# Kernel tuning notes

Hardware: AMD Instinct MI355X
Metric: run time of the kernel (lower is better)

The kernel has to match this reference:

```python
import jax, jax.numpy as jnp
import numpy as np
from jax import lax

# sign binarization to {-1,+1} with straight-through estimator (standard BNN binarizePM1)
@jax.custom_vjp
def binarize(x):
    return jnp.where(x >= 0, 1.0, -1.0).astype(x.dtype)

def _bin_fwd(x):
    return binarize(x), None

def _bin_bwd(_, g):
    return (g,)  # straight-through

binarize.defvjp(_bin_fwd, _bin_bwd)

def conv2d(x, w, b):
    # NCHW, OIHW, 3x3, stride 1, pad 1
    y = lax.conv_general_dilated(x, w, window_strides=(1, 1), padding=((1, 1), (1, 1)),
                                 dimension_numbers=('NCHW', 'OIHW', 'NCHW'))
    return y + b[None, :, None, None]

def maxpool2(x):
    return lax.reduce_window(x, -jnp.inf, lax.max, (1, 1, 2, 2), (1, 1, 2, 2), 'VALID')

def bn(x, gamma, beta, mean, var, eps=1e-5):
    # inference-mode batchnorm; broadcasts over channel axis 1 (4D) or feature axis 1 (2D)
    if x.ndim == 4:
        shp = (1, -1, 1, 1)
    else:
        shp = (1, -1)
    inv = gamma * lax.rsqrt(var + eps)
    return x * inv.reshape(shp) + (beta - mean * inv).reshape(shp)

def setup_inputs() -> dict:
    key = jax.random.key(0)
    ks = jax.random.split(key, 16)
    B = 4096
    d = {}
    d['x'] = jax.random.normal(ks[0], (B, 1, 28, 28), jnp.float32)
    d['conv1_w'] = jax.random.normal(ks[1], (64, 1, 3, 3), jnp.float32) * 0.1
    d['conv1_b'] = jax.random.normal(ks[2], (64,), jnp.float32) * 0.01
    d['conv2_w'] = jax.random.normal(ks[3], (64, 64, 3, 3), jnp.float32) * 0.05
    d['conv2_b'] = jax.random.normal(ks[4], (64,), jnp.float32) * 0.01
    d['fc1_w'] = jax.random.normal(ks[5], (2048, 7 * 7 * 64), jnp.float32) * 0.02
    d['fc1_b'] = jax.random.normal(ks[6], (2048,), jnp.float32) * 0.01
    d['fc2_w'] = jax.random.normal(ks[7], (10, 2048), jnp.float32) * 0.02
    d['fc2_b'] = jax.random.normal(ks[8], (10,), jnp.float32) * 0.01
    for i, (name, c) in enumerate([('bn1', 64), ('bn2', 64), ('bn3', 2048)]):
        d[name + '_gamma'] = jnp.ones((c,), jnp.float32)
        d[name + '_beta'] = jnp.zeros((c,), jnp.float32)
        d[name + '_mean'] = jax.random.normal(ks[9 + i], (c,), jnp.float32) * 0.1
        d[name + '_var'] = jax.random.uniform(ks[12 + i], (c,), jnp.float32, 0.5, 1.5)
    d['scale'] = jnp.array([1e-5], jnp.float32)
    return d

def reference(x, conv1_w, conv1_b, conv2_w, conv2_b, fc1_w, fc1_b, fc2_w, fc2_b,
              bn1_gamma, bn1_beta, bn1_mean, bn1_var,
              bn2_gamma, bn2_beta, bn2_mean, bn2_var,
              bn3_gamma, bn3_beta, bn3_mean, bn3_var, scale):
    h = conv2d(x, binarize(conv1_w), conv1_b)          # [B,64,28,28]
    h = maxpool2(h)                                    # [B,64,14,14]
    h = bn(h, bn1_gamma, bn1_beta, bn1_mean, bn1_var)
    h = jnp.clip(h, -1.0, 1.0)                         # hardtanh
    h = binarize(h)                                    # qact1
    h = conv2d(h, binarize(conv2_w), conv2_b)          # [B,64,14,14]
    h = maxpool2(h)                                    # [B,64,7,7]
    h = bn(h, bn2_gamma, bn2_beta, bn2_mean, bn2_var)
    h = jnp.clip(h, -1.0, 1.0)
    h = binarize(h)
    h = h.reshape(h.shape[0], -1)                      # [B,3136]
    h = h @ binarize(fc1_w).T + fc1_b                  # [B,2048]
    h = bn(h, bn3_gamma, bn3_beta, bn3_mean, bn3_var)
    h = jnp.clip(h, -1.0, 1.0)
    h = binarize(h)
    h = h @ binarize(fc2_w).T + fc2_b                  # [B,10]
    return h * scale
```

## Files before the change

kernel.cpp:

```cpp
#include <hip/hip_runtime.h>
#include <stdint.h>

typedef unsigned long long ULL;

__global__ __launch_bounds__(256) void prep_small(const float* __restrict__ w1,
        const float* __restrict__ w2, const float* __restrict__ fc2w,
        float* __restrict__ sgn1, ULL* __restrict__ wb2, ULL* __restrict__ wbf2) {
    int wave = threadIdx.x >> 6, lane = threadIdx.x & 63;
    int W = blockIdx.x * 4 + wave;
    if (W < 576) {
        int co = W / 9, tap = W - co * 9;
        ULL wd = __ballot(w2[(co * 64 + lane) * 9 + tap] >= 0.f);
        if (lane == 0) wb2[W] = wd;
    } else if (W < 896) {
        int idx = W - 576;
        int n = idx >> 5, k = idx & 31;
        ULL wd = __ballot(fc2w[n * 2048 + k * 64 + lane] >= 0.f);
        if (lane == 0) wbf2[idx] = wd;
    } else if (W < 905) {
        int i = (W - 896) * 64 + lane;
        if (i < 576) sgn1[i] = (w1[i] >= 0.f) ? 1.f : -1.f;
    }
}

__global__ __launch_bounds__(256) void prep_pack_fc1(const float* __restrict__ fc1w,
                                                     ULL* __restrict__ wbT) {
    __shared__ float rows[4 * 3136];
    int t = threadIdx.x;
    const float* src = fc1w + (size_t)blockIdx.x * 4 * 3136;
    for (int i = t; i < 4 * 3136; i += 256) rows[i] = src[i];
    __syncthreads();
    int wave = t >> 6, lane = t & 63;
    int n = blockIdx.x * 4 + wave;
    const float* r = rows + wave * 3136 + lane * 49;
    for (int p = 0; p < 49; ++p) {
        ULL wd = __ballot(r[p] >= 0.f);
        if (lane == 0) wbT[p * 2048 + n] = wd;
    }
}

__global__ __launch_bounds__(448, 4) void k1_conv1(const float* __restrict__ x,
        const float* __restrict__ sgn1, const float* __restrict__ b1,
        const float* __restrict__ g, const float* __restrict__ be,
        const float* __restrict__ mu, const float* __restrict__ va,
        ULL* __restrict__ qact1) {
    __shared__ float limg[30 * 30];
    int b = blockIdx.x, t = threadIdx.x;
    int wave = t >> 6, lane = t & 63;
    for (int i = t; i < 900; i += 448) limg[i] = 0.f;
    __syncthreads();
    const float* xb = x + (size_t)b * 784;
    for (int i = t; i < 784; i += 448) {
        int y = i / 28, xx = i - y * 28;
        limg[(xx + 1) * 30 + (y + 1)] = xb[i];
    }
    float w[9];
    #pragma unroll
    for (int k = 0; k < 9; ++k) w[k] = sgn1[lane * 9 + k];
    double iv = (double)g[lane] / sqrt((double)va[lane] + 1e-5);
    double cd = (double)be[lane] - (double)mu[lane] * iv;
    double bd = (double)b1[lane];
    __syncthreads();

    #pragma unroll
    for (int rr = 0; rr < 2; ++rr) {
        int py = wave + rr * 7;
        const float* base = &limg[2 * py];
        #pragma unroll
        for (int px = 0; px < 14; ++px) {
            float a00 = 0.f, a01 = 0.f, a10 = 0.f, a11 = 0.f;
            #pragma unroll
            for (int ky = 0; ky < 3; ++ky) {
                #pragma unroll
                for (int kx = 0; kx < 3; ++kx) {
                    float sv = w[ky * 3 + kx];
                    a00 = fmaf(base[(2 * px + kx)     * 30 + ky],     sv, a00);
                    a01 = fmaf(base[(2 * px + kx + 1) * 30 + ky],     sv, a01);
                    a10 = fmaf(base[(2 * px + kx)     * 30 + ky + 1], sv, a10);
                    a11 = fmaf(base[(2 * px + kx + 1) * 30 + ky + 1], sv, a11);
                }
            }
            float m = fmaxf(fmaxf(a00, a01), fmaxf(a10, a11));
            double v  = (double)m + bd;
            double tt = v * iv + cd;
            ULL word = __ballot(tt >= 0.0);
            if (lane == 0) qact1[(size_t)b * 196 + py * 14 + px] = word;
        }
    }
}

__global__ __launch_bounds__(256, 1) void k2_conv2(const ULL* __restrict__ qact1,
        const ULL* __restrict__ wb2, const float* __restrict__ b2,
        const float* __restrict__ g, const float* __restrict__ be,
        const float* __restrict__ mu, const float* __restrict__ va,
        ULL* __restrict__ qact2) {
    int lane = threadIdx.x & 63;
    int s = blockIdx.x * 4 + (threadIdx.x >> 6);

    ULL wk[9];
    #pragma unroll
    for (int k = 0; k < 9; ++k) wk[k] = wb2[lane * 9 + k];
    int pw[9];
    #pragma unroll
    for (int k = 0; k < 9; ++k) pw[k] = 64 - 2 * (int)__popcll(wk[k]);

    double iv   = (double)g[lane] / sqrt((double)va[lane] + 1e-5);
    double cc   = (double)be[lane] - (double)mu[lane] * iv;
    double bias = (double)b2[lane];
    int am, thr;
    if (iv > 0.0) {
        double t0 = -cc / iv - bias;
        int c = (t0 < -590.0) ? -590 : (t0 > 590.0 ? 590 : (int)floor(t0) - 2);
        if (c < -590) c = -590;
        while (c <= 590 && !(((double)c + bias) * iv + cc >= 0.0)) ++c;
        am = 1; thr = c;
    } else if (iv < 0.0) {
        double t0 = -cc / iv - bias;
        int c = (t0 > 590.0) ? 590 : (t0 < -590.0 ? -590 : (int)ceil(t0) + 2);
        if (c > 590) c = 590;
        while (c >= -590 && !(((double)c + bias) * iv + cc >= 0.0)) --c;
        am = -1; thr = c;
    } else {
        am = 1; thr = (cc >= 0.0) ? -1000000 : 1000000;
    }
    int athr = am * thr;

    int cLs = pw[0] + pw[3] + pw[6], cRs = pw[2] + pw[5] + pw[8];
    int rT  = pw[0] + pw[1] + pw[2], rB  = pw[6] + pw[7] + pw[8];
    int tL = cLs + rT - pw[0], tM = rT, tR = cRs + rT - pw[2];
    int bL = cLs + rB - pw[6], bM = rB, bR = cRs + rB - pw[8];

    const ULL* base = qact1 + (size_t)s * 196;
    ULL cw[4][4];

    #pragma unroll 1
    for (int pr = 0; pr < 7; ++pr) {
        int r0 = 2 * pr;
        bool tpad = (pr == 0), bpad = (pr == 6);
        const ULL* rA = base + (tpad ? 0 : (r0 - 1) * 14);
        const ULL* rB_ = base + r0 * 14;
        const ULL* rC = base + (r0 + 1) * 14;
        const ULL* rD = base + (bpad ? 0 : (r0 + 2) * 14);
        ULL mT = tpad ? 0ULL : ~0ULL;
        ULL mB = bpad ? 0ULL : ~0ULL;
        int c00 = tpad ? tL : cLs, c01 = tpad ? tM : 0, c02 = tpad ? tR : cRs;
        int c10 = bpad ? bL : cLs, c11 = bpad ? bM : 0, c12 = bpad ? bR : cRs;

        #pragma unroll
        for (int r = 0; r < 4; ++r) cw[0][r] = 0ULL;
        #pragma unroll
        for (int c = 0; c < 3; ++c) {
            cw[c + 1][0] = rA[c] & mT;
            cw[c + 1][1] = rB_[c];
            cw[c + 1][2] = rC[c];
            cw[c + 1][3] = rD[c] & mB;
        }

        #pragma unroll
        for (int px = 0; px < 7; ++px) {
            int s00 = 0, s01 = 0, s10 = 0, s11 = 0;
            #pragma unroll
            for (int ky = 0; ky < 3; ++ky) {
                #pragma unroll
                for (int kx = 0; kx < 3; ++kx) {
                    ULL w = wk[ky * 3 + kx];
                    s00 += (int)__popcll(cw[(2 * px + kx)     & 3][ky    ] ^ w);
                    s01 += (int)__popcll(cw[(2 * px + kx + 1) & 3][ky    ] ^ w);
                    s10 += (int)__popcll(cw[(2 * px + kx)     & 3][ky + 1] ^ w);
                    s11 += (int)__popcll(cw[(2 * px + kx + 1) & 3][ky + 1] ^ w);
                }
            }
            int d00 = 576 - 2 * s00 - ((px == 0) ? c00 : c01);
            int d01 = 576 - 2 * s01 - ((px == 6) ? c02 : c01);
            int d10 = 576 - 2 * s10 - ((px == 0) ? c10 : c11);
            int d11 = 576 - 2 * s11 - ((px == 6) ? c12 : c11);
            int m = max(max(d00, d01), max(d10, d11));
            ULL word = __ballot(am * m >= athr);
            if (lane == 0) qact2[(size_t)s * 49 + pr * 7 + px] = word;

            if (px < 6) {
                const int n1 = 2 * px + 3, n2 = 2 * px + 4;
                cw[(n1 + 1) & 3][0] = rA[n1] & mT;
                cw[(n1 + 1) & 3][1] = rB_[n1];
                cw[(n1 + 1) & 3][2] = rC[n1];
                cw[(n1 + 1) & 3][3] = rD[n1] & mB;
                if (n2 <= 13) {
                    cw[(n2 + 1) & 3][0] = rA[n2] & mT;
                    cw[(n2 + 1) & 3][1] = rB_[n2];
                    cw[(n2 + 1) & 3][2] = rC[n2];
                    cw[(n2 + 1) & 3][3] = rD[n2] & mB;
                } else {
                    #pragma unroll
                    for (int r = 0; r < 4; ++r) cw[(n2 + 1) & 3][r] = 0ULL;
                }
            }
        }
    }
}

__global__ __launch_bounds__(256) void k3_fc1(const ULL* __restrict__ qact2,
        const ULL* __restrict__ wbT, const float* __restrict__ fb,
        const float* __restrict__ g, const float* __restrict__ be,
        const float* __restrict__ mu, const float* __restrict__ va,
        ULL* __restrict__ hbits) {
    __shared__ ULL xs[784];
    int t = threadIdx.x, wave = t >> 6, lane = t & 63;
    int b0 = blockIdx.x * 16;
    int gidx = blockIdx.y * 4 + wave;
    int n = gidx * 64 + lane;
    for (int i = t; i < 784; i += 256) xs[i] = qact2[(size_t)b0 * 49 + i];
    double iv   = (double)g[n] / sqrt((double)va[n] + 1e-5);
    double cc   = (double)be[n] - (double)mu[n] * iv;
    double bias = (double)fb[n];
    __syncthreads();
    int acc[16];
    #pragma unroll
    for (int i = 0; i < 16; ++i) acc[i] = 0;
    for (int p = 0; p < 49; ++p) {
        ULL w = wbT[p * 2048 + n];
        #pragma unroll
        for (int i = 0; i < 16; ++i)
            acc[i] += (int)__popcll(xs[i * 49 + p] ^ w);
    }
    #pragma unroll
    for (int i = 0; i < 16; ++i) {
        int dot = 3136 - 2 * acc[i];
        double tt = ((double)dot + bias) * iv + cc;
        ULL word = __ballot(tt >= 0.0);
        if (lane == 0) hbits[(size_t)(b0 + i) * 32 + gidx] = word;
    }
}

__global__ __launch_bounds__(256) void k4_fc2(const ULL* __restrict__ hbits,
        const ULL* __restrict__ wbf2, const float* __restrict__ b2,
        const float* __restrict__ scale, float* __restrict__ out, int total) {
    int gid = blockIdx.x * 256 + threadIdx.x;
    if (gid >= total) return;
    int b = gid / 10, n = gid - b * 10;
    const ULL* h = hbits + (size_t)b * 32;
    const ULL* w = wbf2 + n * 32;
    int acc = 0;
    #pragma unroll
    for (int k = 0; k < 32; ++k) acc += (int)__popcll(h[k] ^ w[k]);
    int dot = 2048 - 2 * acc;
    double v = ((double)dot + (double)b2[n]) * (double)scale[0];
    out[gid] = (float)v;
}

extern "C" void kernel_launch(void* const* d_in, const int* in_sizes, int n_in,
                              void* d_out, int out_size, void* d_ws, size_t ws_size,
                              hipStream_t stream) {
    const float* x      = (const float*)d_in[0];
    const float* w1     = (const float*)d_in[1];
    const float* b1     = (const float*)d_in[2];
    const float* w2     = (const float*)d_in[3];
    const float* b2     = (const float*)d_in[4];
    const float* fc1w   = (const float*)d_in[5];
    const float* fc1b   = (const float*)d_in[6];
    const float* fc2w   = (const float*)d_in[7];
    const float* fc2b   = (const float*)d_in[8];
    const float* g1 = (const float*)d_in[9],  *be1 = (const float*)d_in[10],
               *mu1 = (const float*)d_in[11], *va1 = (const float*)d_in[12];
    const float* g2 = (const float*)d_in[13], *be2 = (const float*)d_in[14],
               *mu2 = (const float*)d_in[15], *va2 = (const float*)d_in[16];
    const float* g3 = (const float*)d_in[17], *be3 = (const float*)d_in[18],
               *mu3 = (const float*)d_in[19], *va3 = (const float*)d_in[20];
    const float* scale = (const float*)d_in[21];
    float* out = (float*)d_out;

    int B = in_sizes[0] / 784;

    char* ws = (char*)d_ws;
    ULL* qact1 = (ULL*)(ws);
    ULL* qact2 = (ULL*)(ws + (size_t)B * 196 * 8);
    ULL* hbits = (ULL*)(ws + (size_t)B * 245 * 8);
    char* wsw  = ws + (size_t)B * 277 * 8;
    ULL* wb2   = (ULL*)(wsw);
    ULL* wbT   = (ULL*)(wsw + 576 * 8);
    ULL* wbf2  = (ULL*)(wsw + 576 * 8 + 49 * 2048 * 8);
    float* sgn1 = (float*)(wsw + 576 * 8 + 49 * 2048 * 8 + 320 * 8);

    prep_small<<<227, 256, 0, stream>>>(w1, w2, fc2w, sgn1, wb2, wbf2);
    prep_pack_fc1<<<512, 256, 0, stream>>>(fc1w, wbT);

    k1_conv1<<<B, 448, 0, stream>>>(x, sgn1, b1, g1, be1, mu1, va1, qact1);
    k2_conv2<<<B / 4, 256, 0, stream>>>(qact1, wb2, b2, g2, be2, mu2, va2, qact2);
    k3_fc1<<<dim3(B / 16, 8), 256, 0, stream>>>(qact2, wbT, fc1b, g3, be3, mu3, va3, hbits);
    int total = B * 10;
    k4_fc2<<<(total + 255) / 256, 256, 0, stream>>>(hbits, wbf2, fc2b, scale, out, total);
}
```

Measured before the change: 303.2 us.

## Precompute BN sign thresholds and transpose fc1 activation tile for vector LDS reads

Replaces the per-output double-precision batchnorm evaluation in conv1 and fc1 with a per-channel threshold found once at setup. The threshold search steps through float or integer values so the comparison matches the double-precision one exactly. fc1 also stores its shared activation tile transposed so the inner loop reads two 64-bit words per 128-bit LDS load, at the cost of strided global loads when filling the tile. The setup now contains small search loops that may diverge across lanes.

```diff
diff --git a/kernel.cpp b/kernel.cpp
--- a/kernel.cpp
+++ b/kernel.cpp
@@ -1,5 +1,6 @@
 #include <hip/hip_runtime.h>
 #include <stdint.h>
+#include <math.h>
 
 typedef unsigned long long ULL;
 
@@ -60,6 +61,28 @@
     double iv = (double)g[lane] / sqrt((double)va[lane] + 1e-5);
     double cd = (double)be[lane] - (double)mu[lane] * iv;
     double bd = (double)b1[lane];
+    float am, Tf;
+    if (iv > 0.0) {
+        float c = (float)(-cd / iv - bd);
+        for (int it = 0; it < 100 && !(((double)c + bd) * iv + cd >= 0.0); ++it)
+            c = nextafterf(c, 3.4e38f);
+        for (int it = 0; it < 100; ++it) {
+            float d = nextafterf(c, -3.4e38f);
+            if (((double)d + bd) * iv + cd >= 0.0) c = d; else break;
+        }
+        am = 1.f; Tf = c;
+    } else if (iv < 0.0) {
+        float c = (float)(-cd / iv - bd);
+        for (int it = 0; it < 100 && !(((double)c + bd) * iv + cd >= 0.0); ++it)
+            c = nextafterf(c, -3.4e38f);
+        for (int it = 0; it < 100; ++it) {
+            float d = nextafterf(c, 3.4e38f);
+            if (((double)d + bd) * iv + cd >= 0.0) c = d; else break;
+        }
+        am = -1.f; Tf = -c;
+    } else {
+        am = 0.f; Tf = (cd >= 0.0) ? -1.f : 1.f;
+    }
     __syncthreads();
 
     #pragma unroll
@@ -81,9 +104,7 @@
                 }
             }
             float m = fmaxf(fmaxf(a00, a01), fmaxf(a10, a11));
-            double v  = (double)m + bd;
-            double tt = v * iv + cd;
-            ULL word = __ballot(tt >= 0.0);
+            ULL word = __ballot(am * m >= Tf);
             if (lane == 0) qact1[(size_t)b * 196 + py * 14 + px] = word;
         }
     }
@@ -203,15 +224,40 @@
         const float* __restrict__ g, const float* __restrict__ be,
         const float* __restrict__ mu, const float* __restrict__ va,
         ULL* __restrict__ hbits) {
-    __shared__ ULL xs[784];
+    __shared__ __align__(16) ULL xs[784];
     int t = threadIdx.x, wave = t >> 6, lane = t & 63;
     int b0 = blockIdx.x * 16;
     int gidx = blockIdx.y * 4 + wave;
     int n = gidx * 64 + lane;
-    for (int i = t; i < 784; i += 256) xs[i] = qact2[(size_t)b0 * 49 + i];
+    for (int idx = t; idx < 784; idx += 256) {
+        int p = idx >> 4, i = idx & 15;
+        xs[idx] = qact2[(size_t)(b0 + i) * 49 + p];
+    }
     double iv   = (double)g[n] / sqrt((double)va[n] + 1e-5);
     double cc   = (double)be[n] - (double)mu[n] * iv;
     double bias = (double)fb[n];
+    int am, athr;
+    {
+        int amm, thr;
+        if (iv > 0.0) {
+            double t0 = -cc / iv - bias;
+            int c = (t0 < -3200.0) ? -3200 : (t0 > 3200.0 ? 3200 : (int)floor(t0) - 2);
+            if (c < -3200) c = -3200;
+            int it = 0;
+            while (c <= 3200 && !(((double)c + bias) * iv + cc >= 0.0) && it++ < 32) ++c;
+            amm = 1; thr = c;
+        } else if (iv < 0.0) {
+            double t0 = -cc / iv - bias;
+            int c = (t0 > 3200.0) ? 3200 : (t0 < -3200.0 ? -3200 : (int)ceil(t0) + 2);
+            if (c > 3200) c = 3200;
+            int it = 0;
+            while (c >= -3200 && !(((double)c + bias) * iv + cc >= 0.0) && it++ < 32) --c;
+            amm = -1; thr = c;
+        } else {
+            amm = 1; thr = (cc >= 0.0) ? -1000000 : 1000000;
+        }
+        am = amm; athr = amm * thr;
+    }
     __syncthreads();
     int acc[16];
     #pragma unroll
@@ -219,14 +265,16 @@
     for (int p = 0; p < 49; ++p) {
         ULL w = wbT[p * 2048 + n];
         #pragma unroll
-        for (int i = 0; i < 16; ++i)
-            acc[i] += (int)__popcll(xs[i * 49 + p] ^ w);
+        for (int j = 0; j < 8; ++j) {
+            ulonglong2 xv = *(const ulonglong2*)&xs[p * 16 + 2 * j];
+            acc[2 * j]     += (int)__popcll(xv.x ^ w);
+            acc[2 * j + 1] += (int)__popcll(xv.y ^ w);
+        }
     }
     #pragma unroll
     for (int i = 0; i < 16; ++i) {
         int dot = 3136 - 2 * acc[i];
-        double tt = ((double)dot + bias) * iv + cc;
-        ULL word = __ballot(tt >= 0.0);
+        ULL word = __ballot(am * dot >= athr);
         if (lane == 0) hbits[(size_t)(b0 + i) * 32 + gidx] = word;
     }
 }
```

Result: no change. 299.3 us (-1.3%).
